# Optimization experiments

Hardware: AMD Instinct MI355X
Metric: run time of the kernel (lower is better)

The kernel has to match this reference:

```python
import jax, jax.numpy as jnp
import numpy as np

TAU = 20.0
THRESHOLD = 1.0
RESET_V = 0.0
DT = 1.0
SIM_TIME = 100


def setup_inputs() -> dict:
    key = jax.random.key(0)
    ks = jax.random.split(key, 6)
    B, D, H, A = 8192, 256, 256, 64
    return {
        "x": jax.random.normal(ks[0], (B, D), dtype=jnp.float32),
        "enc_W": jax.random.normal(ks[1], (D, D), dtype=jnp.float32) * 0.1,  # Linear weight [out,in]
        "enc_b": jnp.zeros((D,), dtype=jnp.float32),
        "W1": jax.random.normal(ks[2], (D, H), dtype=jnp.float32) * 0.1,
        "W2": jax.random.normal(ks[3], (H, H), dtype=jnp.float32) * 0.1,
        "W3": jax.random.normal(ks[4], (H, A), dtype=jnp.float32) * 0.1,
    }


def _lif_step(v, inp, W, decay):
    # synaptic input -> leaky integrate -> fire -> reset
    syn = inp @ W
    v = v * decay + syn * (1.0 - decay)
    spikes = (v >= THRESHOLD).astype(v.dtype)
    v = jnp.where(spikes > 0, RESET_V, v)
    return v, spikes


def reference(x, enc_W, enc_b, W1, W2, W3):
    B = x.shape[0]
    decay = jnp.exp(jnp.asarray(-DT / TAU, dtype=x.dtype))
    # rate encoding: sigmoid(Linear(x)); constant input at every timestep
    rates = jax.nn.sigmoid(x @ enc_W.T + enc_b)

    H1, H2, A = W1.shape[1], W2.shape[1], W3.shape[1]
    init = (
        jnp.zeros((B, H1), x.dtype),
        jnp.zeros((B, H2), x.dtype),
        jnp.zeros((B, A), x.dtype),
        jnp.zeros((B, A), x.dtype),  # accumulated output spikes
    )

    def step(carry, _):
        v1, v2, v3, acc = carry
        v1, s1 = _lif_step(v1, rates, W1, decay)
        v2, s2 = _lif_step(v2, s1, W2, decay)
        v3, s3 = _lif_step(v3, s2, W3, decay)
        return (v1, v2, v3, acc + s3), None

    (_, _, _, acc), _ = jax.lax.scan(step, init, None, length=SIM_TIME)
    return acc / SIM_TIME
```

## Files before the change

kernel.cpp:

```cpp
#include <hip/hip_runtime.h>
#include <math.h>

#define SIM_T 100

__global__ __launch_bounds__(256) void k_transpose256(
    const float* __restrict__ W, float* __restrict__ WT) {
  int k = blockIdx.x;
  int o = threadIdx.x;
  WT[k * 256 + o] = W[o * 256 + k];
}

__global__ __launch_bounds__(256) void k_perm(const float* __restrict__ W2,
                                              float* __restrict__ W2p) {
  int i = blockIdx.x;
  int t = threadIdx.x;
  int l = t >> 2, q = t & 3;
  W2p[i * 256 + t] = W2[i * 256 + q * 64 + l];
}

template <int EPI>
__global__ __launch_bounds__(256, 4) void k_gemm_rs(
    const float* __restrict__ A,
    const float* __restrict__ WT,
    const float* __restrict__ bias,
    float* __restrict__ O,
    float omd) {
  const int t = threadIdx.x;
  const int lane = t & 63;
  const int w = t >> 6;
  const int rt = blockIdx.x >> 3;
  const int cg = blockIdx.x & 7;
  const int row = rt * 64 + lane;
  const int colbase_v = cg * 32 + w * 8;
  const int colbase = __builtin_amdgcn_readfirstlane(colbase_v);
  const float4* arow4 = (const float4*)(A + (size_t)row * 256);
  const float* wp = WT + colbase;

  float acc[8];
#pragma unroll
  for (int c = 0; c < 8; c++) acc[c] = 0.f;

#pragma unroll
  for (int ph = 0; ph < 4; ph++) {
    float4 a[16];
#pragma unroll
    for (int i = 0; i < 16; i++) a[i] = arow4[ph * 16 + i];
#pragma unroll
    for (int i = 0; i < 16; i++) {
      const float* af = &a[i].x;
#pragma unroll
      for (int kk = 0; kk < 4; kk++) {
        const int k = ph * 64 + i * 4 + kk;
        const float* wk = wp + k * 256;
#pragma unroll
        for (int c = 0; c < 8; c++) acc[c] = fmaf(af[kk], wk[c], acc[c]);
      }
    }
  }

  float* obase = O + (size_t)row * 256 + colbase_v;
  if (EPI == 0) {
    float4 r0, r1;
    float* rf0 = &r0.x;
    float* rf1 = &r1.x;
#pragma unroll
    for (int c = 0; c < 4; c++) {
      float v = acc[c] + bias[colbase + c];
      rf0[c] = 1.f / (1.f + expf(-v));
      float v2 = acc[c + 4] + bias[colbase + c + 4];
      rf1[c] = 1.f / (1.f + expf(-v2));
    }
    *(float4*)obase = r0;
    *(float4*)(obase + 4) = r1;
  } else {
    float4 r0, r1;
    float* rf0 = &r0.x;
    float* rf1 = &r1.x;
#pragma unroll
    for (int c = 0; c < 4; c++) {
      rf0[c] = __fmul_rn(acc[c], omd);
      rf1[c] = __fmul_rn(acc[c + 4], omd);
    }
    *(float4*)obase = r0;
    *(float4*)(obase + 4) = r1;
  }
}

__global__ __launch_bounds__(256, 8) void k_sim(
    const float* __restrict__ c_in, const float* __restrict__ W2p,
    const float* __restrict__ W3, float* __restrict__ out, float decay,
    float omd) {
  const int lane = threadIdx.x & 63;
  const int row = blockIdx.x * 4 + (threadIdx.x >> 6);
  const float* crow = c_in + (long)row * 256;
  const float c0 = crow[lane];
  const float c1 = crow[64 + lane];
  const float c2 = crow[128 + lane];
  const float c3 = crow[192 + lane];
  float v10 = 0.f, v11 = 0.f, v12 = 0.f, v13 = 0.f;
  float v20 = 0.f, v21 = 0.f, v22 = 0.f, v23 = 0.f;
  float v3 = 0.f;
  int acc = 0;
  const float4* w2p = (const float4*)W2p + lane;

  for (int t = 0; t < SIM_T; t++) {
    v10 = __fadd_rn(__fmul_rn(v10, decay), c0);
    bool f0 = v10 >= 1.f;
    unsigned long long m0 = __ballot(f0);
    v10 = f0 ? 0.f : v10;
    v11 = __fadd_rn(__fmul_rn(v11, decay), c1);
    bool f1 = v11 >= 1.f;
    unsigned long long m1 = __ballot(f1);
    v11 = f1 ? 0.f : v11;
    v12 = __fadd_rn(__fmul_rn(v12, decay), c2);
    bool f2 = v12 >= 1.f;
    unsigned long long m2 = __ballot(f2);
    v12 = f2 ? 0.f : v12;
    v13 = __fadd_rn(__fmul_rn(v13, decay), c3);
    bool f3 = v13 >= 1.f;
    unsigned long long m3 = __ballot(f3);
    v13 = f3 ? 0.f : v13;

    float s0 = 0.f, s1 = 0.f, s2 = 0.f, s3 = 0.f;
#define ACC2(mask, qb)                            \
  {                                               \
    unsigned long long m = (mask);                \
    while (m) {                                   \
      int i = __builtin_ctzll(m) + (qb);          \
      m &= m - 1;                                 \
      float4 w = w2p[i * 64];                     \
      s0 += w.x;                                  \
      s1 += w.y;                                  \
      s2 += w.z;                                  \
      s3 += w.w;                                  \
    }                                             \
  }
    ACC2(m0, 0)
    ACC2(m1, 64)
    ACC2(m2, 128)
    ACC2(m3, 192)

    v20 = __fadd_rn(__fmul_rn(v20, decay), __fmul_rn(s0, omd));
    bool g0 = v20 >= 1.f;
    unsigned long long n0 = __ballot(g0);
    v20 = g0 ? 0.f : v20;
    v21 = __fadd_rn(__fmul_rn(v21, decay), __fmul_rn(s1, omd));
    bool g1 = v21 >= 1.f;
    unsigned long long n1 = __ballot(g1);
    v21 = g1 ? 0.f : v21;
    v22 = __fadd_rn(__fmul_rn(v22, decay), __fmul_rn(s2, omd));
    bool g2 = v22 >= 1.f;
    unsigned long long n2 = __ballot(g2);
    v22 = g2 ? 0.f : v22;
    v23 = __fadd_rn(__fmul_rn(v23, decay), __fmul_rn(s3, omd));
    bool g3 = v23 >= 1.f;
    unsigned long long n3 = __ballot(g3);
    v23 = g3 ? 0.f : v23;

    float z = 0.f;
    if (n0 | n1 | n2 | n3) {
#define ACC3(mask, qb)                            \
  {                                               \
    unsigned long long m = (mask);                \
    while (m) {                                   \
      int i = __builtin_ctzll(m) + (qb);          \
      m &= m - 1;                                 \
      z += W3[i * 64 + lane];                     \
    }                                             \
  }
      ACC3(n0, 0)
      ACC3(n1, 64)
      ACC3(n2, 128)
      ACC3(n3, 192)
    }
    v3 = __fadd_rn(__fmul_rn(v3, decay), __fmul_rn(z, omd));
    bool h = v3 >= 1.f;
    acc += h ? 1 : 0;
    v3 = h ? 0.f : v3;
  }
  out[(long)row * 64 + lane] = __fdiv_rn((float)acc, 100.f);
}

extern "C" void kernel_launch(void* const* d_in, const int* in_sizes, int n_in,
                              void* d_out, int out_size, void* d_ws,
                              size_t ws_size, hipStream_t stream) {
  const float* x = (const float*)d_in[0];
  const float* encW = (const float*)d_in[1];
  const float* encB = (const float*)d_in[2];
  const float* W1 = (const float*)d_in[3];
  const float* W2 = (const float*)d_in[4];
  const float* W3 = (const float*)d_in[5];
  float* out = (float*)d_out;

  float* c = (float*)d_ws;
  float* rates = (float*)d_ws + 2097152;
  float* W2p = (float*)d_ws + 4194304;
  float* encWT = (float*)d_ws + 4194304 + 65536;

  const float decay = (float)exp((double)(-0.05f));
  const float omd = 1.0f - decay;

  k_transpose256<<<256, 256, 0, stream>>>(encW, encWT);
  k_perm<<<256, 256, 0, stream>>>(W2, W2p);
  k_gemm_rs<0><<<1024, 256, 0, stream>>>(x, encWT, encB, rates, omd);
  k_gemm_rs<1><<<1024, 256, 0, stream>>>(rates, W1, encB, c, omd);
  k_sim<<<2048, 256, 0, stream>>>(c, W2p, W3, out, decay, omd);
}
```

Before: 205.2 us.

## Restructure encoder and W1 GEMMs so each wave computes 8 rows with broadcast A loads

The two dense GEMMs move from one-row-per-lane tiles to a layout where each wave owns 8 rows and lanes split the 256 output columns in pairs. A values are loaded as wave-uniform addresses, kept uniform through a runtime zero mask so the compiler cannot hoist them to scalar loads, and W rows are read coalesced as float2. The grid is halved and the occupancy hint lowered. The aim is to replace strided per-lane row reads of A with broadcast loads and coalesced weight reads, at the cost of more registers per thread.

Result: slower. 244.7 us (+19.3%).

```diff
diff --git a/kernel.cpp b/kernel.cpp
--- a/kernel.cpp
+++ b/kernel.cpp
@@ -19,70 +19,66 @@
 }
 
 template <int EPI>
-__global__ __launch_bounds__(256, 4) void k_gemm_rs(
+__global__ __launch_bounds__(256, 2) void k_gemm_sv(
     const float* __restrict__ A,
     const float* __restrict__ WT,
     const float* __restrict__ bias,
     float* __restrict__ O,
-    float omd) {
+    float omd, int zero) {
   const int t = threadIdx.x;
   const int lane = t & 63;
-  const int w = t >> 6;
-  const int rt = blockIdx.x >> 3;
-  const int cg = blockIdx.x & 7;
-  const int row = rt * 64 + lane;
-  const int colbase_v = cg * 32 + w * 8;
-  const int colbase = __builtin_amdgcn_readfirstlane(colbase_v);
-  const float4* arow4 = (const float4*)(A + (size_t)row * 256);
-  const float* wp = WT + colbase;
-
-  float acc[8];
-#pragma unroll
-  for (int c = 0; c < 8; c++) acc[c] = 0.f;
-
-#pragma unroll
-  for (int ph = 0; ph < 4; ph++) {
-    float4 a[16];
-#pragma unroll
-    for (int i = 0; i < 16; i++) a[i] = arow4[ph * 16 + i];
-#pragma unroll
-    for (int i = 0; i < 16; i++) {
-      const float* af = &a[i].x;
-#pragma unroll
-      for (int kk = 0; kk < 4; kk++) {
-        const int k = ph * 64 + i * 4 + kk;
-        const float* wk = wp + k * 256;
-#pragma unroll
-        for (int c = 0; c < 8; c++) acc[c] = fmaf(af[kk], wk[c], acc[c]);
-      }
-    }
-  }
-
-  float* obase = O + (size_t)row * 256 + colbase_v;
+  const int wv = t >> 6;
+  const int rg = wv >> 1;
+  const int ch = wv & 1;
+  const int rowbase = blockIdx.x * 16 + rg * 8;
+  const int col = ch * 128 + lane * 2;
+  const float* Ab = A + (size_t)rowbase * 256 + (lane & zero);
+  const float* wp = WT + col;
+
+  float acc[8][2];
+#pragma unroll
+  for (int r = 0; r < 8; r++) acc[r][0] = acc[r][1] = 0.f;
+
+#pragma unroll 2
+  for (int kg = 0; kg < 64; kg++) {
+    float2 w0 = *(const float2*)(wp + (kg * 4 + 0) * 256);
+    float2 w1 = *(const float2*)(wp + (kg * 4 + 1) * 256);
+    float2 w2 = *(const float2*)(wp + (kg * 4 + 2) * 256);
+    float2 w3 = *(const float2*)(wp + (kg * 4 + 3) * 256);
+    float4 a[8];
+#pragma unroll
+    for (int r = 0; r < 8; r++)
+      a[r] = *(const float4*)(Ab + r * 256 + kg * 4);
+#pragma unroll
+    for (int r = 0; r < 8; r++) {
+      acc[r][0] = fmaf(a[r].x, w0.x, acc[r][0]);
+      acc[r][1] = fmaf(a[r].x, w0.y, acc[r][1]);
+      acc[r][0] = fmaf(a[r].y, w1.x, acc[r][0]);
+      acc[r][1] = fmaf(a[r].y, w1.y, acc[r][1]);
+      acc[r][0] = fmaf(a[r].z, w2.x, acc[r][0]);
+      acc[r][1] = fmaf(a[r].z, w2.y, acc[r][1]);
+      acc[r][0] = fmaf(a[r].w, w3.x, acc[r][0]);
+      acc[r][1] = fmaf(a[r].w, w3.y, acc[r][1]);
+    }
+  }
+
   if (EPI == 0) {
-    float4 r0, r1;
-    float* rf0 = &r0.x;
-    float* rf1 = &r1.x;
-#pragma unroll
-    for (int c = 0; c < 4; c++) {
-      float v = acc[c] + bias[colbase + c];
-      rf0[c] = 1.f / (1.f + expf(-v));
-      float v2 = acc[c + 4] + bias[colbase + c + 4];
-      rf1[c] = 1.f / (1.f + expf(-v2));
-    }
-    *(float4*)obase = r0;
-    *(float4*)(obase + 4) = r1;
+    float2 b = *(const float2*)(bias + col);
+#pragma unroll
+    for (int r = 0; r < 8; r++) {
+      float2 o;
+      o.x = 1.f / (1.f + expf(-(acc[r][0] + b.x)));
+      o.y = 1.f / (1.f + expf(-(acc[r][1] + b.y)));
+      *(float2*)(O + (size_t)(rowbase + r) * 256 + col) = o;
+    }
   } else {
-    float4 r0, r1;
-    float* rf0 = &r0.x;
-    float* rf1 = &r1.x;
-#pragma unroll
-    for (int c = 0; c < 4; c++) {
-      rf0[c] = __fmul_rn(acc[c], omd);
-      rf1[c] = __fmul_rn(acc[c + 4], omd);
-    }
-    *(float4*)obase = r0;
-    *(float4*)(obase + 4) = r1;
+#pragma unroll
+    for (int r = 0; r < 8; r++) {
+      float2 o;
+      o.x = __fmul_rn(acc[r][0], omd);
+      o.y = __fmul_rn(acc[r][1], omd);
+      *(float2*)(O + (size_t)(rowbase + r) * 256 + col) = o;
+    }
   }
 }
 
@@ -199,10 +195,11 @@
 
   const float decay = (float)exp((double)(-0.05f));
   const float omd = 1.0f - decay;
+  const int zero = (int)(ws_size & 0);
 
   k_transpose256<<<256, 256, 0, stream>>>(encW, encWT);
   k_perm<<<256, 256, 0, stream>>>(W2, W2p);
-  k_gemm_rs<0><<<1024, 256, 0, stream>>>(x, encWT, encB, rates, omd);
-  k_gemm_rs<1><<<1024, 256, 0, stream>>>(rates, W1, encB, c, omd);
+  k_gemm_sv<0><<<512, 256, 0, stream>>>(x, encWT, encB, rates, omd, zero);
+  k_gemm_sv<1><<<512, 256, 0, stream>>>(rates, W1, encB, c, omd, zero);
   k_sim<<<2048, 256, 0, stream>>>(c, W2p, W3, out, decay, omd);
 }
```
